# Kernel tuning notes

Hardware: AMD Instinct MI355X
Metric: run time of the kernel (lower is better)

Reference implementation:

```python
import jax, jax.numpy as jnp
import numpy as np

H, W, L = 80, 80, 21
NUM_ITERATIONS = 5
ALPHA, BETA, GAMMA = 160.0, 3.0, 3.0  # DenseCRFParams defaults
EPS = 1e-8


def _gaussian_kernel(feats):
    # feats: [N, d] -> K_ij = exp(-0.5 * ||f_i - f_j||^2), symmetric
    sq = jnp.sum(feats * feats, axis=1)
    d2 = sq[:, None] + sq[None, :] - 2.0 * (feats @ feats.T)
    return jnp.exp(-0.5 * jnp.maximum(d2, 0.0))


def _build_filters(image):
    # image: [3, H, W], values in [0, 255]. Lattice features are constants
    # w.r.t. autodiff in the original (custom Function), so stop_gradient.
    img = jax.lax.stop_gradient(image)
    ys, xs = jnp.meshgrid(jnp.arange(H, dtype=jnp.float32),
                          jnp.arange(W, dtype=jnp.float32), indexing="ij")
    pos = jnp.stack([xs.ravel(), ys.ravel()], axis=1)          # [N, 2]
    K_sp = _gaussian_kernel(pos / GAMMA)                        # [N, N]
    rgb = img.reshape(3, -1).T                                  # [N, 3]
    K_bi = _gaussian_kernel(jnp.concatenate([pos / ALPHA, rgb / BETA], axis=1))
    # AbstractFilter normalization: divide by filter applied to all-ones
    norm_sp = 1.0 / (K_sp.sum(axis=1) + EPS)                    # [N]
    norm_bi = 1.0 / (K_bi.sum(axis=1) + EPS)
    return K_sp, norm_sp, K_bi, norm_bi


def setup_inputs() -> dict:
    key = jax.random.key(0)
    k1, k2 = jax.random.split(key)
    image = jax.random.uniform(k1, (1, 3, H, W), dtype=jnp.float32) * 255.0
    logits = jax.random.normal(k2, (1, L, H, W), dtype=jnp.float32)
    eye = jnp.eye(L, dtype=jnp.float32)
    return {
        "image": image,
        "logits": logits,
        "spatial_ker_weights": 3.0 * eye,    # spatial_ker_weight * I
        "bilateral_ker_weights": 5.0 * eye,  # bilateral_ker_weight * I
        "compatibility_matrix": eye,
    }


def reference(image, logits, spatial_ker_weights, bilateral_ker_weights,
              compatibility_matrix):
    img = image[0]          # [3, H, W]
    unary = logits[0].reshape(L, -1)  # [L, N]
    K_sp, norm_sp, K_bi, norm_bi = _build_filters(img)
    cur = unary
    for _ in range(NUM_ITERATIONS):
        q = jax.nn.softmax(cur, axis=0)                  # [L, N]
        # K symmetric: (q @ K)[l, i] = sum_j K_ij q[l, j]
        spatial_out = spatial_ker_weights @ ((q @ K_sp) * norm_sp)
        bilateral_out = bilateral_ker_weights @ ((q @ K_bi) * norm_bi)
        msg = compatibility_matrix @ (spatial_out + bilateral_out)
        cur = msg + unary
    return cur.reshape(1, L, H, W)
```

## Files before the change

kernel.cpp:

```cpp
#include <hip/hip_runtime.h>
#include <hip/hip_bf16.h>
#include <math.h>

#define HH 80
#define WW 80
#define NPIX 6400
#define LL 21
#define NITER 5
#define C_LOG2E 1.44269504088896f

#define SJ  320
#define CHK (SJ / 32)
#define QROW 164
#define QROWS 22
#define NBLK 1000
#define NBY  20
#define NLP  11
#define SPWORK (LL * NPIX)

#define PXB 16
#define SYB (NPIX / PXB)
#define SYT 384

typedef short short8 __attribute__((ext_vector_type(8)));
typedef float f32x16 __attribute__((ext_vector_type(16)));

__device__ inline ushort bf_rne(float x) {
    uint u = __float_as_uint(x);
    return (ushort)((u + 0x7FFFu + ((u >> 16) & 1u)) >> 16);
}
__device__ inline float bf_to_f(ushort h) { return __uint_as_float(((uint)h) << 16); }
__device__ inline uint pk2(float a, float b) {
    __hip_bfloat162 t = __float22bfloat162_rn(make_float2(a, b));
    return *reinterpret_cast<uint*>(&t);
}
__device__ inline uint pk2z(float a, float b) {
    return __builtin_amdgcn_perm(__float_as_uint(b), __float_as_uint(a), 0x07060302u);
}
__device__ inline float fexp2(float x) { return __builtin_amdgcn_exp2f(x); }

__global__ void k_setup(const float* __restrict__ img, const float* __restrict__ unary,
                        const float* __restrict__ Wsp, const float* __restrict__ Wbi,
                        const float* __restrict__ C, ushort* __restrict__ fjg,
                        uint* __restrict__ fig, float* __restrict__ mhs,
                        float* __restrict__ nsp, ushort* __restrict__ qb16,
                        float* __restrict__ M1, float* __restrict__ M2) {
    int tid = threadIdx.x;
    if (blockIdx.x == 25) {
        for (int t = tid; t < LL * LL; t += 256) {
            int l = t / LL, k = t % LL;
            float a = 0.f, b = 0.f;
            for (int m = 0; m < LL; m++) {
                a += C[l * LL + m] * Wsp[m * LL + k];
                b += C[l * LL + m] * Wbi[m * LL + k];
            }
            M1[t] = a; M2[t] = b;
        }
        return;
    }
    __shared__ float sxT[WW];
    if (tid < WW) {
        float s = 0.f;
        for (int t = 0; t < WW; t++) { float d = (float)(tid - t); s += __expf(-d * d * (1.0f / 18.0f)); }
        sxT[tid] = s;
    }
    __syncthreads();
    int i = blockIdx.x * 256 + tid;
    int x = i % WW, y = i / WW;
    float f[5];
    f[0] = (float)x * (1.0f / 160.0f);
    f[1] = (float)y * (1.0f / 160.0f);
    f[2] = (img[0 * NPIX + i] - 127.5f) * (1.0f / 3.0f);
    f[3] = (img[1 * NPIX + i] - 127.5f) * (1.0f / 3.0f);
    f[4] = (img[2 * NPIX + i] - 127.5f) * (1.0f / 3.0f);
    float s = 0.f;
    ushort hi[5], lo[5], Hi[5], Lo[5];
#pragma unroll
    for (int c = 0; c < 5; c++) {
        s += f[c] * f[c];
        hi[c] = bf_rne(f[c]);
        lo[c] = bf_rne(f[c] - bf_to_f(hi[c]));
        float a = C_LOG2E * f[c];
        Hi[c] = bf_rne(a);
        Lo[c] = bf_rne(a - bf_to_f(Hi[c]));
    }
    float mi = -0.5f * C_LOG2E * s;
    mhs[i] = mi;
    ushort mih = bf_rne(mi);
    ushort mil = bf_rne(mi - bf_to_f(mih));
    {
        ushort r0[16] = { hi[0], hi[1], hi[2], hi[3], hi[4], lo[2], lo[3], lo[4],
                          hi[2], hi[3], hi[4], lo[2], lo[3], lo[4], 0x3F80, 0x3F80 };
        uint4 w0, w1;
        w0.x = (uint)r0[0] | ((uint)r0[1] << 16);  w0.y = (uint)r0[2] | ((uint)r0[3] << 16);
        w0.z = (uint)r0[4] | ((uint)r0[5] << 16);  w0.w = (uint)r0[6] | ((uint)r0[7] << 16);
        w1.x = (uint)r0[8] | ((uint)r0[9] << 16);  w1.y = (uint)r0[10] | ((uint)r0[11] << 16);
        w1.z = (uint)r0[12] | ((uint)r0[13] << 16); w1.w = (uint)r0[14] | ((uint)r0[15] << 16);
        *(uint4*)(fjg + (size_t)i * 16) = w0;
        *(uint4*)(fjg + (size_t)i * 16 + 8) = w1;
    }
    {
        ushort r1[16] = { Hi[0], Hi[1], Hi[2], Hi[3], Hi[4], Hi[2], Hi[3], Hi[4],
                          Lo[2], Lo[3], Lo[4], Lo[2], Lo[3], Lo[4], mih, mil };
        uint4 w0, w1;
        w0.x = (uint)r1[0] | ((uint)r1[1] << 16);  w0.y = (uint)r1[2] | ((uint)r1[3] << 16);
        w0.z = (uint)r1[4] | ((uint)r1[5] << 16);  w0.w = (uint)r1[6] | ((uint)r1[7] << 16);
        w1.x = (uint)r1[8] | ((uint)r1[9] << 16);  w1.y = (uint)r1[10] | ((uint)r1[11] << 16);
        w1.z = (uint)r1[12] | ((uint)r1[13] << 16); w1.w = (uint)r1[14] | ((uint)r1[15] << 16);
        *(uint4*)(fig + (size_t)i * 8) = w0;
        *(uint4*)(fig + (size_t)i * 8 + 4) = w1;
    }
    nsp[i] = 1.0f / (sxT[x] * sxT[y] + 1e-8f);
    float v[LL];
    float mx = -1e30f;
    for (int l = 0; l < LL; l++) { v[l] = unary[l * NPIX + i]; mx = fmaxf(mx, v[l]); }
    float ss = 0.f;
    for (int l = 0; l < LL; l++) { v[l] = __expf(v[l] - mx); ss += v[l]; }
    float r = 1.0f / ss;
    for (int l = 0; l < LL; l++) qb16[(size_t)l * NPIX + i] = bf_rne(v[l] * r);
}

__device__ inline f32x16 ldmhs(const float* p, int h) {
    float4 a0 = *(const float4*)(p + 8 * h);
    float4 a1 = *(const float4*)(p + 8 * h + 4);
    float4 a2 = *(const float4*)(p + 16 + 8 * h);
    float4 a3 = *(const float4*)(p + 16 + 8 * h + 4);
    f32x16 cv;
    cv[0] = a0.x;  cv[1] = a0.y;  cv[2] = a0.z;  cv[3] = a0.w;
    cv[4] = a1.x;  cv[5] = a1.y;  cv[6] = a1.z;  cv[7] = a1.w;
    cv[8] = a2.x;  cv[9] = a2.y;  cv[10] = a2.z; cv[11] = a2.w;
    cv[12] = a3.x; cv[13] = a3.y; cv[14] = a3.z; cv[15] = a3.w;
    return cv;
}

__global__ __launch_bounds__(256, 4)
void k_iter1(const float* __restrict__ mhs, const ushort* __restrict__ fjg,
             const uint* __restrict__ fig, const ushort* __restrict__ qb16,
             uint* __restrict__ bip, float* __restrict__ tmpx) {
    __shared__ __align__(16) uint  FjL[SJ * 12];
    __shared__ __align__(16) float mhsL[SJ];
    __shared__ __align__(16) uint  QL[QROWS * QROW];
    __shared__ float gT[WW];
    int tid = threadIdx.x;
    int bid = blockIdx.x;
    int bx = bid % 50, by = bid / 50;
    int j0 = by * SJ;
    for (int idx = tid; idx < QROWS * (SJ / 2); idx += 256) {
        int l = idx / (SJ / 2), jp = idx % (SJ / 2);
        uint v;
        if (l < LL) {
            const uint* p = (const uint*)qb16 + (((size_t)l * NPIX + j0) >> 1);
            v = p[jp];
        } else {
            v = 0x3F803F80u;
        }
        QL[l * QROW + jp] = v;
    }
    for (int idx = tid; idx < SJ * 2; idx += 256) {
        int r = idx >> 1, hf = idx & 1;
        uint4 v = ((const uint4*)(fjg + (size_t)(j0 + r) * 16))[hf];
        *(uint4*)&FjL[r * 12 + hf * 4] = v;
    }
    for (int idx = tid; idx < SJ; idx += 256) mhsL[idx] = mhs[j0 + idx];
    if (tid < WW) gT[tid] = __expf(-(float)(tid * tid) * (1.0f / 18.0f));
    int lane = tid & 63, wid = tid >> 6;
    int h = lane >> 5, m = lane & 31;
    int i = bx * 128 + wid * 32 + m;
    union U8 { uint u[4]; short8 s; };
    U8 bfr;
    {
        uint4 bv = *(const uint4*)(fig + (size_t)i * 8 + h * 4);
        bfr.u[0] = bv.x; bfr.u[1] = bv.y; bfr.u[2] = bv.z; bfr.u[3] = bv.w;
    }
    int jrow = (m & ~12) | ((m & 4) << 1) | ((m & 8) >> 1);
    int qrow = (m < QROWS) ? m : 0;
    __syncthreads();
    f32x16 acc;
#pragma unroll
    for (int k = 0; k < 16; k++) acc[k] = 0.f;
    const uint* qbase = &QL[qrow * QROW + h * 4];
    for (int c = 0; c < CHK; c++) {
        int jb = c * 32;
        f32x16 cv = ldmhs(&mhsL[jb], h);
        short8 af = *(const short8*)&FjL[(jb + jrow) * 12 + h * 4];
        f32x16 d1 = __builtin_amdgcn_mfma_f32_32x32x16_bf16(af, bfr.s, cv, 0, 0, 0);
        short8 qa = *(const short8*)(qbase + c * 16);
        short8 qb = *(const short8*)(qbase + c * 16 + 8);
        U8 ea;
        ea.u[0] = pk2z(fexp2(d1[0]), fexp2(d1[1]));
        ea.u[1] = pk2z(fexp2(d1[2]), fexp2(d1[3]));
        ea.u[2] = pk2z(fexp2(d1[4]), fexp2(d1[5]));
        ea.u[3] = pk2z(fexp2(d1[6]), fexp2(d1[7]));
        acc = __builtin_amdgcn_mfma_f32_32x32x16_bf16(qa, ea.s, acc, 0, 0, 0);
        U8 eb;
        eb.u[0] = pk2z(fexp2(d1[8]),  fexp2(d1[9]));
        eb.u[1] = pk2z(fexp2(d1[10]), fexp2(d1[11]));
        eb.u[2] = pk2z(fexp2(d1[12]), fexp2(d1[13]));
        eb.u[3] = pk2z(fexp2(d1[14]), fexp2(d1[15]));
        acc = __builtin_amdgcn_mfma_f32_32x32x16_bf16(qb, eb.s, acc, 0, 0, 0);
    }
#pragma unroll
    for (int r = 0; r < 16; r += 2) {
        int l = (r & 3) + 8 * (r >> 2) + 4 * h;
        if (l < LL + 1)
            bip[((size_t)by * NLP + (l >> 1)) * NPIX + i] = pk2(acc[r], acc[r + 1]);
    }
    {
        int start = (int)(((long)bid * SPWORK) / NBLK);
        int end   = (int)(((long)(bid + 1) * SPWORK) / NBLK);
        int cnt = end - start;
        if (tid < cnt) {
            int fidx = start + tid;
            int l = fidx / NPIX;
            int p = fidx - l * NPIX;
            int x = p % WW, y = p / WW;
            const ushort* rowq = qb16 + (size_t)l * NPIX + y * WW;
            float s = 0.f;
            for (int xp = 0; xp < WW; xp++) {
                int d = x - xp; d = d < 0 ? -d : d;
                s += gT[d] * bf_to_f(rowq[xp]);
            }
            tmpx[(size_t)l * NPIX + p] = s;
        }
    }
}

__global__ __launch_bounds__(SYT)
void k_syc(const float* __restrict__ unary, const float* __restrict__ tmpx,
           const uint* __restrict__ bip, const float* __restrict__ nsp,
           const float* __restrict__ M1, const float* __restrict__ M2,
           ushort* __restrict__ qb16, float* __restrict__ out, int last) {
    __shared__ float m1s[LL * 24];
    __shared__ float m2s[LL * 24];
    __shared__ float gT[HH];
    __shared__ float svL[PXB][QROWS];
    __shared__ float bvL[PXB][QROWS];
    __shared__ float aex[PXB][QROWS];
    int tid = threadIdx.x;
    int px0 = blockIdx.x * PXB;
    for (int t = tid; t < LL * LL; t += SYT) {
        int l = t / LL, k = t % LL;
        m1s[l * 24 + k] = M1[t];
        m2s[l * 24 + k] = M2[t];
    }
    if (tid < HH) gT[tid] = __expf(-(float)(tid * tid) * (1.0f / 18.0f));
    __syncthreads();
    if (tid < PXB * LL) {
        int pxl = tid & (PXB - 1);
        int l = tid >> 4;
        int px = px0 + pxl;
        int x = px % WW, y = px / WW;
        const float* base = tmpx + (size_t)l * NPIX + x;
        float s1 = 0.f;
        for (int yp = 0; yp < HH; yp++) {
            int d = y - yp; d = d < 0 ? -d : d;
            s1 += gT[d] * base[yp * WW];
        }
        svL[pxl][l] = s1;
    }
    if (tid < PXB * NLP) {
        int pxl = tid & (PXB - 1);
        int lp = tid >> 4;
        int px = px0 + pxl;
        float sa = 0.f, sb = 0.f;
        const uint* p = bip + (size_t)lp * NPIX + px;
#pragma unroll
        for (int byi = 0; byi < NBY; byi++) {
            uint v = p[(size_t)byi * NLP * NPIX];
            sa += __uint_as_float(v << 16);
            sb += __uint_as_float(v & 0xFFFF0000u);
        }
        bvL[pxl][2 * lp] = sa;
        bvL[pxl][2 * lp + 1] = sb;
    }
    __syncthreads();
    if (tid < PXB * LL) {
        int pxl = tid & (PXB - 1);
        int l = tid >> 4;
        int px = px0 + pxl;
        float ns = nsp[px];
        float nb = 1.0f / (bvL[pxl][LL] + 1e-8f);
        float s1 = 0.f, s2 = 0.f;
        const float* r1 = &m1s[l * 24];
        const float* r2 = &m2s[l * 24];
#pragma unroll
        for (int k = 0; k < LL; k++) {
            s1 = fmaf(r1[k], svL[pxl][k], s1);
            s2 = fmaf(r2[k], bvL[pxl][k], s2);
        }
        float a = unary[l * NPIX + px] + ns * s1 + nb * s2;
        if (last) out[(size_t)l * NPIX + px] = a;
        else      aex[pxl][l] = a;
    }
    if (last) return;
    __syncthreads();
    if (tid < PXB) {
        int px = px0 + tid;
        float mx = -1e30f;
        for (int l = 0; l < LL; l++) mx = fmaxf(mx, aex[tid][l]);
        float s = 0.f;
        float e[LL];
        for (int l = 0; l < LL; l++) { e[l] = __expf(aex[tid][l] - mx); s += e[l]; }
        float r = 1.0f / s;
        for (int l = 0; l < LL; l++)
            qb16[(size_t)l * NPIX + px] = bf_rne(e[l] * r);
    }
}

extern "C" void kernel_launch(void* const* d_in, const int* in_sizes, int n_in,
                              void* d_out, int out_size, void* d_ws, size_t ws_size,
                              hipStream_t stream) {
    const float* img   = (const float*)d_in[0];
    const float* unary = (const float*)d_in[1];
    const float* Wsp   = (const float*)d_in[2];
    const float* Wbi   = (const float*)d_in[3];
    const float* C     = (const float*)d_in[4];
    float* out = (float*)d_out;

    const int LN = LL * NPIX;
    float* w = (float*)d_ws;
    float*  tmpx = w;  w += LN;
    uint*   bip  = (uint*)w;    w += NBY * NLP * NPIX;
    float*  mhs  = w;  w += NPIX;
    float*  nsp  = w;  w += NPIX;
    ushort* fjg  = (ushort*)w;  w += 8 * NPIX;
    uint*   fig  = (uint*)w;    w += 8 * NPIX;
    ushort* qb16 = (ushort*)w;  w += (LN + 1) / 2;
    float*  M1   = w;  w += LL * LL;
    float*  M2   = w;  w += LL * LL;

    k_setup<<<26, 256, 0, stream>>>(img, unary, Wsp, Wbi, C, fjg, fig, mhs, nsp,
                                    qb16, M1, M2);
    for (int it = 0; it < NITER; it++) {
        int last = (it == NITER - 1);
        k_iter1<<<NBLK, 256, 0, stream>>>(mhs, fjg, fig, qb16, bip, tmpx);
        k_syc<<<SYB, SYT, 0, stream>>>(unary, tmpx, bip, nsp, M1, M2, qb16, out, last);
    }
}
```

Before: 190.2 us.

## Swizzle LDS layouts, pre-permute mhs in global, widen sync kernel blocks

Stores the per-pixel mhs values in a pre-permuted global layout so the MFMA accumulator init reads them directly as float4 from global/L1 instead of staging them through shared memory. Applies an XOR swizzle to the Q and feature tiles in LDS and loads Q with uint4 instead of single uints, aiming to cut bank conflicts and load instruction count. The sync kernel now handles 32 pixels per block with 1024 threads, and its column-sum and bilateral partial-sum reductions run on disjoint thread ranges so they execute concurrently. Setup is split into 51 blocks of 128 active threads. The extra global loads inside the hot loop and the larger blocks may cost occupancy.

```diff
diff --git a/kernel.cpp b/kernel.cpp
--- a/kernel.cpp
+++ b/kernel.cpp
@@ -18,9 +18,9 @@
 #define NLP  11
 #define SPWORK (LL * NPIX)
 
-#define PXB 16
+#define PXB 32
 #define SYB (NPIX / PXB)
-#define SYT 384
+#define SYT 1024
 
 typedef short short8 __attribute__((ext_vector_type(8)));
 typedef float f32x16 __attribute__((ext_vector_type(16)));
@@ -42,11 +42,11 @@
 __global__ void k_setup(const float* __restrict__ img, const float* __restrict__ unary,
                         const float* __restrict__ Wsp, const float* __restrict__ Wbi,
                         const float* __restrict__ C, ushort* __restrict__ fjg,
-                        uint* __restrict__ fig, float* __restrict__ mhs,
+                        uint* __restrict__ fig, float* __restrict__ mhs2,
                         float* __restrict__ nsp, ushort* __restrict__ qb16,
                         float* __restrict__ M1, float* __restrict__ M2) {
     int tid = threadIdx.x;
-    if (blockIdx.x == 25) {
+    if (blockIdx.x == 50) {
         for (int t = tid; t < LL * LL; t += 256) {
             int l = t / LL, k = t % LL;
             float a = 0.f, b = 0.f;
@@ -65,7 +65,8 @@
         sxT[tid] = s;
     }
     __syncthreads();
-    int i = blockIdx.x * 256 + tid;
+    if (tid >= 128) return;
+    int i = blockIdx.x * 128 + tid;
     int x = i % WW, y = i / WW;
     float f[5];
     f[0] = (float)x * (1.0f / 160.0f);
@@ -85,7 +86,11 @@
         Lo[c] = bf_rne(a - bf_to_f(Hi[c]));
     }
     float mi = -0.5f * C_LOG2E * s;
-    mhs[i] = mi;
+    {
+        int r = i & 31;
+        int pos = (r & 7) | ((r & 8) << 1) | ((r & 16) >> 1);
+        mhs2[(size_t)(i >> 5) * 32 + pos] = mi;
+    }
     ushort mih = bf_rne(mi);
     ushort mil = bf_rne(mi - bf_to_f(mih));
     {
@@ -120,48 +125,32 @@
     for (int l = 0; l < LL; l++) qb16[(size_t)l * NPIX + i] = bf_rne(v[l] * r);
 }
 
-__device__ inline f32x16 ldmhs(const float* p, int h) {
-    float4 a0 = *(const float4*)(p + 8 * h);
-    float4 a1 = *(const float4*)(p + 8 * h + 4);
-    float4 a2 = *(const float4*)(p + 16 + 8 * h);
-    float4 a3 = *(const float4*)(p + 16 + 8 * h + 4);
-    f32x16 cv;
-    cv[0] = a0.x;  cv[1] = a0.y;  cv[2] = a0.z;  cv[3] = a0.w;
-    cv[4] = a1.x;  cv[5] = a1.y;  cv[6] = a1.z;  cv[7] = a1.w;
-    cv[8] = a2.x;  cv[9] = a2.y;  cv[10] = a2.z; cv[11] = a2.w;
-    cv[12] = a3.x; cv[13] = a3.y; cv[14] = a3.z; cv[15] = a3.w;
-    return cv;
-}
-
 __global__ __launch_bounds__(256, 4)
-void k_iter1(const float* __restrict__ mhs, const ushort* __restrict__ fjg,
+void k_iter1(const float* __restrict__ mhs2, const ushort* __restrict__ fjg,
              const uint* __restrict__ fig, const ushort* __restrict__ qb16,
              uint* __restrict__ bip, float* __restrict__ tmpx) {
     __shared__ __align__(16) uint  FjL[SJ * 12];
-    __shared__ __align__(16) float mhsL[SJ];
     __shared__ __align__(16) uint  QL[QROWS * QROW];
     __shared__ float gT[WW];
     int tid = threadIdx.x;
     int bid = blockIdx.x;
     int bx = bid % 50, by = bid / 50;
     int j0 = by * SJ;
-    for (int idx = tid; idx < QROWS * (SJ / 2); idx += 256) {
-        int l = idx / (SJ / 2), jp = idx % (SJ / 2);
-        uint v;
+    for (int idx = tid; idx < QROWS * 40; idx += 256) {
+        int l = idx / 40, u = idx - l * 40;
+        uint4 v;
         if (l < LL) {
-            const uint* p = (const uint*)qb16 + (((size_t)l * NPIX + j0) >> 1);
-            v = p[jp];
+            v = *((const uint4*)(qb16 + ((size_t)l * NPIX + j0)) + u);
         } else {
-            v = 0x3F803F80u;
-        }
-        QL[l * QROW + jp] = v;
+            v.x = 0x3F803F80u; v.y = 0x3F803F80u; v.z = 0x3F803F80u; v.w = 0x3F803F80u;
+        }
+        *(uint4*)&QL[l * QROW + ((u ^ ((l >> 3) & 1)) << 2)] = v;
     }
     for (int idx = tid; idx < SJ * 2; idx += 256) {
         int r = idx >> 1, hf = idx & 1;
         uint4 v = ((const uint4*)(fjg + (size_t)(j0 + r) * 16))[hf];
-        *(uint4*)&FjL[r * 12 + hf * 4] = v;
-    }
-    for (int idx = tid; idx < SJ; idx += 256) mhsL[idx] = mhs[j0 + idx];
+        *(uint4*)&FjL[r * 12 + ((hf ^ ((r >> 3) & 1)) << 2)] = v;
+    }
     if (tid < WW) gT[tid] = __expf(-(float)(tid * tid) * (1.0f / 18.0f));
     int lane = tid & 63, wid = tid >> 6;
     int h = lane >> 5, m = lane & 31;
@@ -173,19 +162,30 @@
         bfr.u[0] = bv.x; bfr.u[1] = bv.y; bfr.u[2] = bv.z; bfr.u[3] = bv.w;
     }
     int jrow = (m & ~12) | ((m & 4) << 1) | ((m & 8) >> 1);
+    int xf = (jrow >> 3) & 1;
     int qrow = (m < QROWS) ? m : 0;
+    int xq = (qrow >> 3) & 1;
+    const uint* qlbase = &QL[qrow * QROW];
+    const float4* mbase = (const float4*)(mhs2 + (size_t)(j0 >> 5) * 32) + h * 4;
     __syncthreads();
     f32x16 acc;
 #pragma unroll
     for (int k = 0; k < 16; k++) acc[k] = 0.f;
-    const uint* qbase = &QL[qrow * QROW + h * 4];
     for (int c = 0; c < CHK; c++) {
         int jb = c * 32;
-        f32x16 cv = ldmhs(&mhsL[jb], h);
-        short8 af = *(const short8*)&FjL[(jb + jrow) * 12 + h * 4];
+        f32x16 cv;
+        {
+            const float4* mc = mbase + c * 8;
+            float4 a0 = mc[0], a1 = mc[1], a2 = mc[2], a3 = mc[3];
+            cv[0] = a0.x;  cv[1] = a0.y;  cv[2] = a0.z;  cv[3] = a0.w;
+            cv[4] = a1.x;  cv[5] = a1.y;  cv[6] = a1.z;  cv[7] = a1.w;
+            cv[8] = a2.x;  cv[9] = a2.y;  cv[10] = a2.z; cv[11] = a2.w;
+            cv[12] = a3.x; cv[13] = a3.y; cv[14] = a3.z; cv[15] = a3.w;
+        }
+        short8 af = *(const short8*)&FjL[(jb + jrow) * 12 + ((h ^ xf) << 2)];
         f32x16 d1 = __builtin_amdgcn_mfma_f32_32x32x16_bf16(af, bfr.s, cv, 0, 0, 0);
-        short8 qa = *(const short8*)(qbase + c * 16);
-        short8 qb = *(const short8*)(qbase + c * 16 + 8);
+        short8 qa = *(const short8*)(qlbase + (((c * 4 + h) ^ xq) << 2));
+        short8 qb = *(const short8*)(qlbase + (((c * 4 + 2 + h) ^ xq) << 2));
         U8 ea;
         ea.u[0] = pk2z(fexp2(d1[0]), fexp2(d1[1]));
         ea.u[1] = pk2z(fexp2(d1[2]), fexp2(d1[3]));
@@ -247,7 +247,7 @@
     __syncthreads();
     if (tid < PXB * LL) {
         int pxl = tid & (PXB - 1);
-        int l = tid >> 4;
+        int l = tid / PXB;
         int px = px0 + pxl;
         int x = px % WW, y = px / WW;
         const float* base = tmpx + (size_t)l * NPIX + x;
@@ -257,26 +257,28 @@
             s1 += gT[d] * base[yp * WW];
         }
         svL[pxl][l] = s1;
-    }
-    if (tid < PXB * NLP) {
-        int pxl = tid & (PXB - 1);
-        int lp = tid >> 4;
-        int px = px0 + pxl;
-        float sa = 0.f, sb = 0.f;
-        const uint* p = bip + (size_t)lp * NPIX + px;
-#pragma unroll
-        for (int byi = 0; byi < NBY; byi++) {
-            uint v = p[(size_t)byi * NLP * NPIX];
-            sa += __uint_as_float(v << 16);
-            sb += __uint_as_float(v & 0xFFFF0000u);
-        }
-        bvL[pxl][2 * lp] = sa;
-        bvL[pxl][2 * lp + 1] = sb;
+    } else {
+        int t2 = tid - PXB * LL;
+        if (t2 < PXB * NLP) {
+            int pxl = t2 & (PXB - 1);
+            int lp = t2 / PXB;
+            int px = px0 + pxl;
+            float sa = 0.f, sb = 0.f;
+            const uint* p = bip + (size_t)lp * NPIX + px;
+#pragma unroll
+            for (int byi = 0; byi < NBY; byi++) {
+                uint v = p[(size_t)byi * NLP * NPIX];
+                sa += __uint_as_float(v << 16);
+                sb += __uint_as_float(v & 0xFFFF0000u);
+            }
+            bvL[pxl][2 * lp] = sa;
+            bvL[pxl][2 * lp + 1] = sb;
+        }
     }
     __syncthreads();
     if (tid < PXB * LL) {
         int pxl = tid & (PXB - 1);
-        int l = tid >> 4;
+        int l = tid / PXB;
         int px = px0 + pxl;
         float ns = nsp[px];
         float nb = 1.0f / (bvL[pxl][LL] + 1e-8f);
@@ -321,7 +323,7 @@
     float* w = (float*)d_ws;
     float*  tmpx = w;  w += LN;
     uint*   bip  = (uint*)w;    w += NBY * NLP * NPIX;
-    float*  mhs  = w;  w += NPIX;
+    float*  mhs2 = w;  w += NPIX;
     float*  nsp  = w;  w += NPIX;
     ushort* fjg  = (ushort*)w;  w += 8 * NPIX;
     uint*   fig  = (uint*)w;    w += 8 * NPIX;
@@ -329,11 +331,11 @@
     float*  M1   = w;  w += LL * LL;
     float*  M2   = w;  w += LL * LL;
 
-    k_setup<<<26, 256, 0, stream>>>(img, unary, Wsp, Wbi, C, fjg, fig, mhs, nsp,
+    k_setup<<<51, 256, 0, stream>>>(img, unary, Wsp, Wbi, C, fjg, fig, mhs2, nsp,
                                     qb16, M1, M2);
     for (int it = 0; it < NITER; it++) {
         int last = (it == NITER - 1);
-        k_iter1<<<NBLK, 256, 0, stream>>>(mhs, fjg, fig, qb16, bip, tmpx);
+        k_iter1<<<NBLK, 256, 0, stream>>>(mhs2, fjg, fig, qb16, bip, tmpx);
         k_syc<<<SYB, SYT, 0, stream>>>(unary, tmpx, bip, nsp, M1, M2, qb16, out, last);
     }
 }
```

New measurement: 175.8 us. -7.6%, faster.
